# Kernel tuning notes

Hardware: AMD Instinct MI355X
Metric: run time of the kernel (lower is better)

## Reference

```python
import jax, jax.numpy as jnp
import numpy as np

HID = 64      # HIDDEN_DIM
VOCAB = 64    # VOCAB_SIZE
INNER = 24    # INNER_DIM
SEQ = 32      # SEQ_LEN
CAP = 8       # CAPACITY_LIMIT (deque maxlen)
LR = 0.05     # INFERENCE_LR
B1, B2, EPS = 0.9, 0.999, 1e-8   # torch Adam defaults
LN_EPS = 1e-5                    # torch LayerNorm default
BATCH = 8192


def setup_inputs() -> dict:
    key = jax.random.key(0)
    ks = jax.random.split(key, 8)
    def w(k, shape, s=0.02):
        return jax.random.normal(k, shape, jnp.float32) * s
    return {
        "seqs": jax.random.randint(ks[0], (BATCH, SEQ), 0, VOCAB, dtype=jnp.int32),
        "embed": w(ks[1], (VOCAB, HID), 1.0),
        "ff_w1": w(ks[2], (HID, 2 * HID)), "ff_b1": jnp.zeros((2 * HID,), jnp.float32),
        "ff_w2": w(ks[3], (2 * HID, HID)), "ff_b2": jnp.zeros((HID,), jnp.float32),
        "ln_g": jnp.ones((HID,), jnp.float32), "ln_b": jnp.zeros((HID,), jnp.float32),
        "mlp_w1": w(ks[4], (HID, INNER), 0.1), "mlp_b1": jnp.zeros((INNER,), jnp.float32),
        "mlp_w2": w(ks[5], (INNER, HID), 0.1), "mlp_b2": jnp.zeros((HID,), jnp.float32),
        "out_w": w(ks[6], (HID, VOCAB)), "out_b": jnp.zeros((VOCAB,), jnp.float32),
    }


def _mlp(p, x):
    w1, b1, w2, b2 = p
    return jnp.maximum(x @ w1 + b1, 0.0) @ w2 + b2


def reference(seqs, embed, ff_w1, ff_b1, ff_w2, ff_b2, ln_g, ln_b,
              mlp_w1, mlp_b1, mlp_w2, mlp_b2, out_w, out_b):
    # Encoder over all tokens used (t = 0..SEQ-2), batched: [B, 31, HID]
    h = embed[seqs[:, : SEQ - 1]]
    f = jnp.maximum(h @ ff_w1 + ff_b1, 0.0) @ ff_w2 + ff_b2
    x = h + f
    mu = x.mean(-1, keepdims=True)
    var = ((x - mu) ** 2).mean(-1, keepdims=True)
    enc = ln_g * (x - mu) * jax.lax.rsqrt(var + LN_EPS) + ln_b

    # deque(maxlen=8) over pairs (t even -> key, t odd -> val) keeps last 8 pairs:
    # keys at t = 14,16,...,28 ; vals at t = 15,17,...,29. Entries are detached.
    keys = jax.lax.stop_gradient(enc[:, 14:29:2])  # [B, 8, HID]
    vals = jax.lax.stop_gradient(enc[:, 15:30:2])  # [B, 8, HID]
    q = enc[:, SEQ - 2]                            # [B, HID]

    # load_state_dict copy breaks the graph -> base MLP params are constants here
    p0 = tuple(jax.lax.stop_gradient(p) for p in (mlp_w1, mlp_b1, mlp_w2, mlp_b2))
    steps = jnp.arange(1, CAP + 1, dtype=jnp.float32)

    def per_sample(k_i, v_i, q_i):
        def adam_step(carry, kv):
            p, m, v = carry
            kh, vh, t = kv
            g = jax.grad(lambda pp: jnp.mean((_mlp(pp, kh) - vh) ** 2))(p)
            m = jax.tree_util.tree_map(lambda a, b: B1 * a + (1.0 - B1) * b, m, g)
            v = jax.tree_util.tree_map(lambda a, b: B2 * a + (1.0 - B2) * b * b, v, g)
            bc1 = 1.0 - B1 ** t
            bc2 = 1.0 - B2 ** t
            p = jax.tree_util.tree_map(
                lambda pp, mm, vv: pp - LR * (mm / bc1) / (jnp.sqrt(vv / bc2) + EPS),
                p, m, v)
            return (p, m, v), None
        zeros = jax.tree_util.tree_map(jnp.zeros_like, p0)
        (pT, _, _), _ = jax.lax.scan(adam_step, (p0, zeros, zeros), (k_i, v_i, steps))
        return _mlp(pT, q_i)

    hq = jax.vmap(per_sample)(keys, vals, q)   # [B, HID]
    return hq @ out_w + out_b                  # [B, VOCAB]
```

## Files before the change

### kernel.cpp

```cpp
#include <hip/hip_runtime.h>
#include <hip/hip_bf16.h>
#include <math.h>

#define HID   64
#define VOCABN 64
#define INNER 24
#define SEQN  32
#define CAPN  8
#define NPOS  17
#define BATCHN 8192

typedef float f32x4 __attribute__((ext_vector_type(4)));

static __device__ const float CMSBR[8] = {
  0.01581139f, 0.01176584f, 0.01010053f, 0.00918844f,
  0.00862495f, 0.00825540f, 0.00800653f, 0.00783856f
};

__device__ __forceinline__ float allred64(float x) {
  int y;
  y = __builtin_amdgcn_update_dpp(__float_as_int(x), __float_as_int(x),
                                  0xB1, 0xF, 0xF, false);
  x += __int_as_float(y);
  y = __builtin_amdgcn_update_dpp(__float_as_int(x), __float_as_int(x),
                                  0x4E, 0xF, 0xF, false);
  x += __int_as_float(y);
  x += __int_as_float(__builtin_amdgcn_ds_swizzle(__float_as_int(x), 0x101F));
  x += __int_as_float(__builtin_amdgcn_ds_swizzle(__float_as_int(x), 0x201F));
  x += __int_as_float(__builtin_amdgcn_ds_swizzle(__float_as_int(x), 0x401F));
  x += __shfl_xor(x, 32);
  return x;
}

__global__ __launch_bounds__(128) void build_table(
    const float* __restrict__ embed,
    const float* __restrict__ ff_w1,
    const float* __restrict__ ff_b1,
    const float* __restrict__ ff_w2,
    const float* __restrict__ ff_b2,
    const float* __restrict__ ln_g,
    const float* __restrict__ ln_b,
    float* __restrict__ etab)
{
  __shared__ float h[64];
  __shared__ float A1[128];
  __shared__ float xs[64];
  const int r = blockIdx.x;
  const int t = threadIdx.x;

  if (t < 64) h[t] = embed[r * 64 + t];
  __syncthreads();

  {
    float acc = ff_b1[t];
    #pragma unroll 8
    for (int k = 0; k < 64; ++k)
      acc = fmaf(h[k], ff_w1[k * 128 + t], acc);
    A1[t] = fmaxf(acc, 0.f);
  }
  __syncthreads();

  if (t < 64) {
    float acc = ff_b2[t];
    #pragma unroll 8
    for (int k = 0; k < 128; ++k)
      acc = fmaf(A1[k], ff_w2[k * 64 + t], acc);
    xs[t] = acc + h[t];
  }
  __syncthreads();

  if (t < 64) {
    float s1 = 0.f;
    if (t < 4)
      for (int j = 0; j < 16; ++j) s1 += xs[t + 4 * j];
    s1 += __shfl_xor(s1, 1);
    s1 += __shfl_xor(s1, 2);
    s1 = __shfl(s1, 0);
    float mu = s1 * 0.015625f;

    float s2 = 0.f;
    if (t < 4)
      for (int j = 0; j < 16; ++j) {
        float d = xs[t + 4 * j] - mu;
        s2 = fmaf(d, d, s2);
      }
    s2 += __shfl_xor(s2, 1);
    s2 += __shfl_xor(s2, 2);
    s2 = __shfl(s2, 0);
    float var = s2 * 0.015625f;
    float rs  = rsqrtf(var + 1e-5f);

    etab[r * 64 + t] = fmaf((xs[t] - mu) * rs, ln_g[t], ln_b[t]);
  }
}

__device__ __forceinline__ void adam_upd(float& p, float& m, float& v,
                                         float g1, float g2, float cmsbr) {
  m = fmaf(0.9f, m, g1);
  v = fmaf(0.999f, v, g2);
  p = fmaf(-(m * cmsbr), __builtin_amdgcn_rsqf(fmaxf(v, 1e-30f)), p);
}

__global__ __launch_bounds__(128, 3) void adapt_kernel(
    const int* __restrict__ seqs,
    const float* __restrict__ etab,
    const float* __restrict__ mlp_w1,
    const float* __restrict__ mlp_b1,
    const float* __restrict__ mlp_w2,
    const float* __restrict__ mlp_b2,
    const float* __restrict__ out_w,
    const float* __restrict__ out_b,
    float* __restrict__ out)
{
  __shared__ float ybuf[2][2][64];
  __shared__ float hqv[64];
  const int t    = threadIdx.x;
  const int lane = t & 63;
  const int w    = t >> 6;
  const int s    = blockIdx.x;
  const int i0   = 12 * w;

  int tok = (lane < NPOS) ? seqs[s * SEQN + 14 + lane] : 0;

  float w1r[12], m1[12], v1[12], w2c[12], m2[12], v2[12];
  #pragma unroll
  for (int i = 0; i < 12; ++i) {
    w1r[i] = mlp_w1[lane * 24 + i0 + i];
    w2c[i] = mlp_w2[(i0 + i) * 64 + lane];
    m1[i] = 0.f; v1[i] = 0.f; m2[i] = 0.f; v2[i] = 0.f;
  }
  float b1o = (lane < 12) ? mlp_b1[i0 + lane] : 0.f;
  float b2o = (w == 0) ? mlp_b2[lane] : 0.f;
  float mb1 = 0.f, vb1 = 0.f, mb2 = 0.f, vb2 = 0.f;

  int tk = __shfl(tok, 0), tv = __shfl(tok, 1);
  float kj = etab[tk * 64 + lane];
  float vj = etab[tv * 64 + lane];

  #pragma unroll 1
  for (int st = 0; st < 8; ++st) {
    const float cmsbr = CMSBR[st];

    float zp[12];
    #pragma unroll
    for (int i = 0; i < 12; ++i) zp[i] = kj * w1r[i];
    #pragma unroll
    for (int i = 0; i < 12; ++i) zp[i] += (lane == i) ? b1o : 0.f;
    #pragma unroll
    for (int i = 0; i < 12; ++i) zp[i] = allred64(zp[i]);

    float a[12];
    #pragma unroll
    for (int i = 0; i < 12; ++i) a[i] = fmaxf(zp[i], 0.f);

    float yp = (w == 0) ? b2o : 0.f;
    #pragma unroll
    for (int i = 0; i < 12; ++i) yp = fmaf(a[i], w2c[i], yp);
    ybuf[st & 1][w][lane] = yp;
    __syncthreads();
    float y = ybuf[st & 1][0][lane] + ybuf[st & 1][1][lane];
    float dy = (y - vj) * 0.03125f;

    int p1 = 2 * st + 2; p1 = p1 < 16 ? p1 : 16;
    int p2 = 2 * st + 3; p2 = p2 < 16 ? p2 : 16;
    int tk2 = __shfl(tok, p1), tv2 = __shfl(tok, p2);
    float kn = etab[tk2 * 64 + lane];
    float vn = etab[tv2 * 64 + lane];

    float dz[12];
    #pragma unroll
    for (int i = 0; i < 12; ++i) dz[i] = w2c[i] * dy;
    #pragma unroll
    for (int i = 0; i < 12; ++i) dz[i] = allred64(dz[i]);
    #pragma unroll
    for (int i = 0; i < 12; ++i) dz[i] = (a[i] > 0.f) ? dz[i] : 0.f;

    float kj01 = 0.1f   * kj;
    float kjsq = 0.001f * kj * kj;
    float dy01 = 0.1f   * dy;
    float dysq = 0.001f * dy * dy;
    #pragma unroll
    for (int i = 0; i < 12; ++i)
      adam_upd(w1r[i], m1[i], v1[i], kj01 * dz[i], kjsq * (dz[i] * dz[i]), cmsbr);
    #pragma unroll
    for (int i = 0; i < 12; ++i)
      adam_upd(w2c[i], m2[i], v2[i], dy01 * a[i], dysq * (a[i] * a[i]), cmsbr);
    adam_upd(b2o, mb2, vb2, dy01, dysq, cmsbr);
    float gb1 = 0.f;
    #pragma unroll
    for (int i = 0; i < 12; ++i) gb1 = (lane == i) ? dz[i] : gb1;
    adam_upd(b1o, mb1, vb1, 0.1f * gb1, 0.001f * (gb1 * gb1), cmsbr);

    kj = kn; vj = vn;
  }

  float zq[12];
  #pragma unroll
  for (int i = 0; i < 12; ++i) zq[i] = kj * w1r[i];
  #pragma unroll
  for (int i = 0; i < 12; ++i) zq[i] += (lane == i) ? b1o : 0.f;
  #pragma unroll
  for (int i = 0; i < 12; ++i) zq[i] = allred64(zq[i]);
  float hp = (w == 0) ? b2o : 0.f;
  #pragma unroll
  for (int i = 0; i < 12; ++i) hp = fmaf(fmaxf(zq[i], 0.f), w2c[i], hp);

  ybuf[0][w][lane] = hp;
  __syncthreads();
  hqv[lane] = ybuf[0][0][lane] + ybuf[0][1][lane];
  __syncthreads();

  if (w == 0) {
    float acc = out_b[lane];
    const f32x4* hv = (const f32x4*)hqv;
    #pragma unroll
    for (int j4 = 0; j4 < 16; ++j4) {
      f32x4 h4 = hv[j4];
      acc = fmaf(h4.x, out_w[(4 * j4 + 0) * 64 + lane], acc);
      acc = fmaf(h4.y, out_w[(4 * j4 + 1) * 64 + lane], acc);
      acc = fmaf(h4.z, out_w[(4 * j4 + 2) * 64 + lane], acc);
      acc = fmaf(h4.w, out_w[(4 * j4 + 3) * 64 + lane], acc);
    }
    out[(size_t)s * 64 + lane] = acc;
  }
}

extern "C" void kernel_launch(void* const* d_in, const int* in_sizes, int n_in,
                              void* d_out, int out_size, void* d_ws, size_t ws_size,
                              hipStream_t stream) {
  const int*   seqs   = (const int*)d_in[0];
  const float* embed  = (const float*)d_in[1];
  const float* ff_w1  = (const float*)d_in[2];
  const float* ff_b1  = (const float*)d_in[3];
  const float* ff_w2  = (const float*)d_in[4];
  const float* ff_b2  = (const float*)d_in[5];
  const float* ln_g   = (const float*)d_in[6];
  const float* ln_b   = (const float*)d_in[7];
  const float* mlp_w1 = (const float*)d_in[8];
  const float* mlp_b1 = (const float*)d_in[9];
  const float* mlp_w2 = (const float*)d_in[10];
  const float* mlp_b2 = (const float*)d_in[11];
  const float* out_w  = (const float*)d_in[12];
  const float* out_b  = (const float*)d_in[13];

  float* etab = (float*)d_ws;

  build_table<<<64, 128, 0, stream>>>(
      embed, ff_w1, ff_b1, ff_w2, ff_b2, ln_g, ln_b, etab);
  adapt_kernel<<<BATCHN, 128, 0, stream>>>(
      seqs, etab, mlp_w1, mlp_b1, mlp_w2, mlp_b2, out_w, out_b,
      (float*)d_out);
}
```

Before: 208.2 us.

## Split each wave into two half-waves over inner units, reducing within 32 lanes

Each 64-lane wave now treats its halves as separate groups. Each half owns 6 of the 24 inner units, and each lane holds two hidden dimensions loaded as float2. This drops the cross-32 shuffle from every reduction and halves the number of reductions per lane, at the cost of a second FMA per partial product and a four-way partial-sum combine through shared memory. Bias ownership and the updates to the b1 and b2 Adam state are remapped to match the new lane layout.

After: 182.4 us. 1.14x faster.

```diff
diff --git a/kernel.cpp b/kernel.cpp
--- a/kernel.cpp
+++ b/kernel.cpp
@@ -17,7 +17,7 @@
   0.00862495f, 0.00825540f, 0.00800653f, 0.00783856f
 };
 
-__device__ __forceinline__ float allred64(float x) {
+__device__ __forceinline__ float allred32(float x) {
   int y;
   y = __builtin_amdgcn_update_dpp(__float_as_int(x), __float_as_int(x),
                                   0xB1, 0xF, 0xF, false);
@@ -28,7 +28,6 @@
   x += __int_as_float(__builtin_amdgcn_ds_swizzle(__float_as_int(x), 0x101F));
   x += __int_as_float(__builtin_amdgcn_ds_swizzle(__float_as_int(x), 0x201F));
   x += __int_as_float(__builtin_amdgcn_ds_swizzle(__float_as_int(x), 0x401F));
-  x += __shfl_xor(x, 32);
   return x;
 }
 
@@ -112,102 +111,147 @@
     const float* __restrict__ out_b,
     float* __restrict__ out)
 {
-  __shared__ float ybuf[2][2][64];
-  __shared__ float hqv[64];
+  __shared__ float2 yb[2][2][2][32];
+  __shared__ __align__(16) float hqv[64];
   const int t    = threadIdx.x;
   const int lane = t & 63;
   const int w    = t >> 6;
+  const int h    = lane >> 5;
+  const int u    = lane & 31;
   const int s    = blockIdx.x;
-  const int i0   = 12 * w;
+  const int off  = 12 * w + 6 * h;
 
   int tok = (lane < NPOS) ? seqs[s * SEQN + 14 + lane] : 0;
 
-  float w1r[12], m1[12], v1[12], w2c[12], m2[12], v2[12];
+  float w1a[6], w1b[6], m1a[6], v1a[6], m1b[6], v1b[6];
+  float w2a[6], w2b[6], m2a[6], v2a[6], m2b[6], v2b[6];
   #pragma unroll
-  for (int i = 0; i < 12; ++i) {
-    w1r[i] = mlp_w1[lane * 24 + i0 + i];
-    w2c[i] = mlp_w2[(i0 + i) * 64 + lane];
-    m1[i] = 0.f; v1[i] = 0.f; m2[i] = 0.f; v2[i] = 0.f;
-  }
-  float b1o = (lane < 12) ? mlp_b1[i0 + lane] : 0.f;
-  float b2o = (w == 0) ? mlp_b2[lane] : 0.f;
-  float mb1 = 0.f, vb1 = 0.f, mb2 = 0.f, vb2 = 0.f;
-
+  for (int m = 0; m < 6; ++m) {
+    w1a[m] = mlp_w1[(2 * u)     * INNER + off + m];
+    w1b[m] = mlp_w1[(2 * u + 1) * INNER + off + m];
+    w2a[m] = mlp_w2[(off + m) * HID + 2 * u];
+    w2b[m] = mlp_w2[(off + m) * HID + 2 * u + 1];
+    m1a[m] = v1a[m] = m1b[m] = v1b[m] = 0.f;
+    m2a[m] = v2a[m] = m2b[m] = v2b[m] = 0.f;
+  }
+  const int  d    = u - 3 * h;
+  const bool own1 = ((unsigned)d < 3u);
+  float b1lo = own1 ? mlp_b1[off + 2 * d]     : 0.f;
+  float b1hi = own1 ? mlp_b1[off + 2 * d + 1] : 0.f;
+  float mb1l = 0.f, vb1l = 0.f, mb1h = 0.f, vb1h = 0.f;
+  const bool w0h0 = (w == 0) && (h == 0);
+  float b2lo = w0h0 ? mlp_b2[2 * u]     : 0.f;
+  float b2hi = w0h0 ? mlp_b2[2 * u + 1] : 0.f;
+  float mb2l = 0.f, vb2l = 0.f, mb2h = 0.f, vb2h = 0.f;
+
+  const bool o0 = (u == 3 * h);
+  const bool o1 = (u == 3 * h + 1);
+  const bool o2 = (u == 3 * h + 2);
+
+  const float2* e2 = (const float2*)etab;
   int tk = __shfl(tok, 0), tv = __shfl(tok, 1);
-  float kj = etab[tk * 64 + lane];
-  float vj = etab[tv * 64 + lane];
+  float2 kp = e2[tk * 32 + u];
+  float2 vp = e2[tv * 32 + u];
 
   #pragma unroll 1
   for (int st = 0; st < 8; ++st) {
     const float cmsbr = CMSBR[st];
 
-    float zp[12];
-    #pragma unroll
-    for (int i = 0; i < 12; ++i) zp[i] = kj * w1r[i];
-    #pragma unroll
-    for (int i = 0; i < 12; ++i) zp[i] += (lane == i) ? b1o : 0.f;
-    #pragma unroll
-    for (int i = 0; i < 12; ++i) zp[i] = allred64(zp[i]);
-
-    float a[12];
-    #pragma unroll
-    for (int i = 0; i < 12; ++i) a[i] = fmaxf(zp[i], 0.f);
-
-    float yp = (w == 0) ? b2o : 0.f;
-    #pragma unroll
-    for (int i = 0; i < 12; ++i) yp = fmaf(a[i], w2c[i], yp);
-    ybuf[st & 1][w][lane] = yp;
+    float p0[6], p1[6];
+    #pragma unroll
+    for (int m = 0; m < 6; ++m) { p0[m] = kp.x * w1a[m]; p1[m] = kp.y * w1b[m]; }
+    p0[0] += o0 ? b1lo : 0.f;  p1[1] += o0 ? b1hi : 0.f;
+    p0[2] += o1 ? b1lo : 0.f;  p1[3] += o1 ? b1hi : 0.f;
+    p0[4] += o2 ? b1lo : 0.f;  p1[5] += o2 ? b1hi : 0.f;
+    float a[6];
+    #pragma unroll
+    for (int m = 0; m < 6; ++m) a[m] = allred32(p0[m] + p1[m]);
+    #pragma unroll
+    for (int m = 0; m < 6; ++m) a[m] = fmaxf(a[m], 0.f);
+
+    float yp0 = w0h0 ? b2lo : 0.f;
+    float yp1 = w0h0 ? b2hi : 0.f;
+    #pragma unroll
+    for (int m = 0; m < 6; ++m) {
+      yp0 = fmaf(a[m], w2a[m], yp0);
+      yp1 = fmaf(a[m], w2b[m], yp1);
+    }
+    yb[st & 1][w][h][u] = make_float2(yp0, yp1);
     __syncthreads();
-    float y = ybuf[st & 1][0][lane] + ybuf[st & 1][1][lane];
-    float dy = (y - vj) * 0.03125f;
-
-    int p1 = 2 * st + 2; p1 = p1 < 16 ? p1 : 16;
-    int p2 = 2 * st + 3; p2 = p2 < 16 ? p2 : 16;
-    int tk2 = __shfl(tok, p1), tv2 = __shfl(tok, p2);
-    float kn = etab[tk2 * 64 + lane];
-    float vn = etab[tv2 * 64 + lane];
-
-    float dz[12];
-    #pragma unroll
-    for (int i = 0; i < 12; ++i) dz[i] = w2c[i] * dy;
-    #pragma unroll
-    for (int i = 0; i < 12; ++i) dz[i] = allred64(dz[i]);
-    #pragma unroll
-    for (int i = 0; i < 12; ++i) dz[i] = (a[i] > 0.f) ? dz[i] : 0.f;
-
-    float kj01 = 0.1f   * kj;
-    float kjsq = 0.001f * kj * kj;
-    float dy01 = 0.1f   * dy;
-    float dysq = 0.001f * dy * dy;
-    #pragma unroll
-    for (int i = 0; i < 12; ++i)
-      adam_upd(w1r[i], m1[i], v1[i], kj01 * dz[i], kjsq * (dz[i] * dz[i]), cmsbr);
-    #pragma unroll
-    for (int i = 0; i < 12; ++i)
-      adam_upd(w2c[i], m2[i], v2[i], dy01 * a[i], dysq * (a[i] * a[i]), cmsbr);
-    adam_upd(b2o, mb2, vb2, dy01, dysq, cmsbr);
-    float gb1 = 0.f;
-    #pragma unroll
-    for (int i = 0; i < 12; ++i) gb1 = (lane == i) ? dz[i] : gb1;
-    adam_upd(b1o, mb1, vb1, 0.1f * gb1, 0.001f * (gb1 * gb1), cmsbr);
-
-    kj = kn; vj = vn;
-  }
-
-  float zq[12];
-  #pragma unroll
-  for (int i = 0; i < 12; ++i) zq[i] = kj * w1r[i];
-  #pragma unroll
-  for (int i = 0; i < 12; ++i) zq[i] += (lane == i) ? b1o : 0.f;
-  #pragma unroll
-  for (int i = 0; i < 12; ++i) zq[i] = allred64(zq[i]);
-  float hp = (w == 0) ? b2o : 0.f;
-  #pragma unroll
-  for (int i = 0; i < 12; ++i) hp = fmaf(fmaxf(zq[i], 0.f), w2c[i], hp);
-
-  ybuf[0][w][lane] = hp;
-  __syncthreads();
-  hqv[lane] = ybuf[0][0][lane] + ybuf[0][1][lane];
+    float2 q00 = yb[st & 1][0][0][u];
+    float2 q01 = yb[st & 1][0][1][u];
+    float2 q10 = yb[st & 1][1][0][u];
+    float2 q11 = yb[st & 1][1][1][u];
+    float y0  = (q00.x + q01.x) + (q10.x + q11.x);
+    float y1  = (q00.y + q01.y) + (q10.y + q11.y);
+    float dy0 = (y0 - vp.x) * 0.03125f;
+    float dy1 = (y1 - vp.y) * 0.03125f;
+
+    int pp1 = 2 * st + 2; pp1 = pp1 < 16 ? pp1 : 16;
+    int pp2 = 2 * st + 3; pp2 = pp2 < 16 ? pp2 : 16;
+    int tk2 = __shfl(tok, pp1), tv2 = __shfl(tok, pp2);
+    float2 kn = e2[tk2 * 32 + u];
+    float2 vn = e2[tv2 * 32 + u];
+
+    float dz[6];
+    #pragma unroll
+    for (int m = 0; m < 6; ++m) {
+      float b0 = w2a[m] * dy0;
+      float b1 = w2b[m] * dy1;
+      dz[m] = allred32(b0 + b1);
+    }
+    #pragma unroll
+    for (int m = 0; m < 6; ++m) dz[m] = (a[m] > 0.f) ? dz[m] : 0.f;
+
+    float k001  = 0.1f   * kp.x,        k101  = 0.1f   * kp.y;
+    float k0s   = 0.001f * kp.x * kp.x, k1s   = 0.001f * kp.y * kp.y;
+    float dy001 = 0.1f   * dy0,         dy101 = 0.1f   * dy1;
+    float dy0s  = 0.001f * dy0 * dy0,   dy1s  = 0.001f * dy1 * dy1;
+    #pragma unroll
+    for (int m = 0; m < 6; ++m) {
+      float dzs = dz[m] * dz[m];
+      adam_upd(w1a[m], m1a[m], v1a[m], k001 * dz[m], k0s * dzs, cmsbr);
+      adam_upd(w1b[m], m1b[m], v1b[m], k101 * dz[m], k1s * dzs, cmsbr);
+      float as = a[m] * a[m];
+      adam_upd(w2a[m], m2a[m], v2a[m], dy001 * a[m], dy0s * as, cmsbr);
+      adam_upd(w2b[m], m2b[m], v2b[m], dy101 * a[m], dy1s * as, cmsbr);
+    }
+    float glo = o0 ? dz[0] : (o1 ? dz[2] : dz[4]);
+    float ghi = o0 ? dz[1] : (o1 ? dz[3] : dz[5]);
+    adam_upd(b1lo, mb1l, vb1l, 0.1f * glo, 0.001f * (glo * glo), cmsbr);
+    adam_upd(b1hi, mb1h, vb1h, 0.1f * ghi, 0.001f * (ghi * ghi), cmsbr);
+    if (w == 0) {
+      adam_upd(b2lo, mb2l, vb2l, dy001, dy0s, cmsbr);
+      adam_upd(b2hi, mb2h, vb2h, dy101, dy1s, cmsbr);
+    }
+
+    kp = kn; vp = vn;
+  }
+
+  {
+    float p0[6], p1[6];
+    #pragma unroll
+    for (int m = 0; m < 6; ++m) { p0[m] = kp.x * w1a[m]; p1[m] = kp.y * w1b[m]; }
+    p0[0] += o0 ? b1lo : 0.f;  p1[1] += o0 ? b1hi : 0.f;
+    p0[2] += o1 ? b1lo : 0.f;  p1[3] += o1 ? b1hi : 0.f;
+    p0[4] += o2 ? b1lo : 0.f;  p1[5] += o2 ? b1hi : 0.f;
+    float hp0 = w0h0 ? b2lo : 0.f;
+    float hp1 = w0h0 ? b2hi : 0.f;
+    #pragma unroll
+    for (int m = 0; m < 6; ++m) {
+      float aq = fmaxf(allred32(p0[m] + p1[m]), 0.f);
+      hp0 = fmaf(aq, w2a[m], hp0);
+      hp1 = fmaf(aq, w2b[m], hp1);
+    }
+    yb[0][w][h][u] = make_float2(hp0, hp1);
+  }
+  __syncthreads();
+  if (t < 32) {
+    float2 f00 = yb[0][0][0][u], f01 = yb[0][0][1][u];
+    float2 f10 = yb[0][1][0][u], f11 = yb[0][1][1][u];
+    ((float2*)hqv)[u] = make_float2((f00.x + f01.x) + (f10.x + f11.x),
+                                    (f00.y + f01.y) + (f10.y + f11.y));
+  }
   __syncthreads();
 
   if (w == 0) {
```
